# Kernel optimization log

Hardware: AMD Instinct MI355X
Metric: run time of the kernel (lower is better)

## Reference

```python
import jax, jax.numpy as jnp
from jax import lax
import numpy as np

B, T, D, H, C = 256, 2048, 40, 128, 35
LN_EPS = 1e-5


def _uniform(key, shape, scale):
    return jax.random.uniform(key, shape, jnp.float32, -scale, scale)


def setup_inputs() -> dict:
    key = jax.random.key(0)
    ks = jax.random.split(key, 16)
    s = 1.0 / np.sqrt(H)  # PyTorch LSTM init scale
    inp = {
        "x": jax.random.normal(ks[0], (B, T, D), jnp.float32),
        "length": jax.random.randint(ks[1], (B,), 1, T + 1, jnp.int32),
        # layer 0 (input_size=D)
        "W_ih0": _uniform(ks[2], (4 * H, D), s),
        "W_hh0": _uniform(ks[3], (4 * H, H), s),
        "b_ih0": _uniform(ks[4], (4 * H,), s),
        "b_hh0": _uniform(ks[5], (4 * H,), s),
        # layer 1 (input_size=H)
        "W_ih1": _uniform(ks[6], (4 * H, H), s),
        "W_hh1": _uniform(ks[7], (4 * H, H), s),
        "b_ih1": _uniform(ks[8], (4 * H,), s),
        "b_hh1": _uniform(ks[9], (4 * H,), s),
        # LayerNorm + Linear head
        "ln_gamma": jnp.ones((H,), jnp.float32),
        "ln_beta": jnp.zeros((H,), jnp.float32),
        "fc_w": _uniform(ks[10], (C, H), 1.0 / np.sqrt(H)),
        "fc_b": _uniform(ks[11], (C,), 1.0 / np.sqrt(H)),
    }
    return inp


def _lstm_layer(xs, length, W_ih, W_hh, b_ih, b_hh):
    # xs: [T, B, D_in]; masked recurrence emulates pack_padded_sequence:
    # state is frozen for t >= length, so the final h equals the state at
    # each sequence's last valid step.
    Tn, Bn = xs.shape[0], xs.shape[1]
    Hn = W_hh.shape[1]
    h0 = jnp.zeros((Bn, Hn), xs.dtype)
    c0 = jnp.zeros((Bn, Hn), xs.dtype)

    def step(carry, inp):
        h, c = carry
        x_t, t = inp
        gates = x_t @ W_ih.T + b_ih + h @ W_hh.T + b_hh  # [B, 4H]
        i, f, g, o = jnp.split(gates, 4, axis=-1)  # PyTorch gate order i,f,g,o
        i = jax.nn.sigmoid(i)
        f = jax.nn.sigmoid(f)
        g = jnp.tanh(g)
        o = jax.nn.sigmoid(o)
        c_new = f * c + i * g
        h_new = o * jnp.tanh(c_new)
        m = (t < length)[:, None]
        h = jnp.where(m, h_new, h)
        c = jnp.where(m, c_new, c)
        return (h, c), h

    (h_fin, c_fin), hs = lax.scan(step, (h0, c0), (xs, jnp.arange(Tn)))
    return hs, h_fin


def reference(x, length, W_ih0, W_hh0, b_ih0, b_hh0, W_ih1, W_hh1, b_ih1, b_hh1,
              ln_gamma, ln_beta, fc_w, fc_b):
    xs = jnp.transpose(x, (1, 0, 2))  # [T, B, D]
    hs1, _ = _lstm_layer(xs, length, W_ih0, W_hh0, b_ih0, b_hh0)
    _, h_last = _lstm_layer(hs1, length, W_ih1, W_hh1, b_ih1, b_hh1)  # h[-1]: [B, H]
    # LayerNorm over feature dim
    mu = jnp.mean(h_last, axis=-1, keepdims=True)
    var = jnp.mean(jnp.square(h_last - mu), axis=-1, keepdims=True)
    hn = (h_last - mu) * lax.rsqrt(var + LN_EPS) * ln_gamma + ln_beta
    return hn @ fc_w.T + fc_b  # [B, C]
```

## Files before the change

### kernel.cpp

```cpp
#include <hip/hip_runtime.h>

#define Bn 256
#define Tn 2048
#define Dn 40
#define Hn 128
#define Cn 35

typedef _Float16 h2 __attribute__((ext_vector_type(2)));

__device__ __forceinline__ int sdot4(int a, int b, int c) {
#if __has_builtin(__builtin_amdgcn_sdot4)
  return __builtin_amdgcn_sdot4(a, b, c, false);
#else
  int r = c;
#pragma unroll
  for (int i = 0; i < 4; ++i)
    r += ((int)(a << (24 - 8 * i)) >> 24) * ((int)(b << (24 - 8 * i)) >> 24);
  return r;
#endif
}

__device__ __forceinline__ float fdot2f(h2 a, h2 b, float c) {
#if __has_builtin(__builtin_amdgcn_fdot2)
  return __builtin_amdgcn_fdot2(a, b, c, false);
#else
  return c + (float)(a[0]) * (float)(b[0]) + (float)(a[1]) * (float)(b[1]);
#endif
}

__device__ __forceinline__ h2 bch(int u) { return __builtin_bit_cast(h2, u); }

__device__ __forceinline__ int pk2i(float a, float b) {
  h2 r; r[0] = (_Float16)a; r[1] = (_Float16)b;
  return __builtin_bit_cast(int, r);
}

__device__ __forceinline__ float rcpf_(float x) {
#if __has_builtin(__builtin_amdgcn_rcpf)
  return __builtin_amdgcn_rcpf(x);
#else
  return 1.f / x;
#endif
}

__device__ __forceinline__ float sigm(float v) {
  v = fmaxf(fminf(v, 60.f), -60.f);
  return rcpf_(1.f + __expf(-v));
}

__device__ __forceinline__ float tanha(float v) {
  v = fmaxf(fminf(v, 15.f), -15.f);
  const float e = __expf(2.f * v);
  return (e - 1.f) * rcpf_(e + 1.f);
}

__device__ __forceinline__ int q8c(float v) {
  v = fminf(fmaxf(v, -127.f), 127.f);
  return (int)__builtin_rintf(v);
}

__device__ __forceinline__ int pk4(int a, int b, int c, int d) {
  return (a & 255) | ((b & 255) << 8) | ((c & 255) << 16) | (d << 24);
}

__device__ __forceinline__ int dpp_x1(int v) {
  return __builtin_amdgcn_update_dpp(0, v, 0xB1, 0xF, 0xF, true);
}
__device__ __forceinline__ int dpp_x2(int v) {
  return __builtin_amdgcn_update_dpp(0, v, 0x4E, 0xF, 0xF, true);
}

#if __has_builtin(__builtin_amdgcn_global_load_lds)
#define HAVE_GLDS 1
__device__ __forceinline__ void gl_lds16(const float* g, float* l) {
  __builtin_amdgcn_global_load_lds(
      (const __attribute__((address_space(1))) unsigned int*)(const void*)g,
      (__attribute__((address_space(3))) unsigned int*)(void*)l, 16, 0, 0);
}
#endif

__device__ __forceinline__ void quantW128(const float* __restrict__ p,
                                          int* __restrict__ q, float& sc) {
  float m = 1e-30f;
#pragma unroll
  for (int i = 0; i < 32; ++i) {
    const float4 v = reinterpret_cast<const float4*>(p)[i];
    m = fmaxf(m, fmaxf(fmaxf(fabsf(v.x), fabsf(v.y)),
                       fmaxf(fabsf(v.z), fabsf(v.w))));
  }
  const float inv = 127.f / m;
  sc = m * (1.f / 127.f);
#pragma unroll
  for (int i = 0; i < 32; ++i) {
    const float4 v = reinterpret_cast<const float4*>(p)[i];
    q[i] = pk4(q8c(v.x * inv), q8c(v.y * inv), q8c(v.z * inv), q8c(v.w * inv));
  }
}

#define RLST(w) __builtin_amdgcn_readlane(                                  \
    ((w) < 64 ? st0 : (w) < 128 ? st1 : (w) < 192 ? st2 : (w) < 256 ? st3  \
                                                        : st4), (w) & 63)

#define MEMBAR() asm volatile("" ::: "memory")
#define POLL_GE(idx, val, cache)                                             \
  do {                                                                       \
    if ((cache) < (val)) {                                                   \
      do { (cache) = *(volatile int*)&s_flag[idx]; } while ((cache) < (val));\
    }                                                                        \
    MEMBAR();                                                                \
  } while (0)
#define PUBLISH(idx, val)                                                    \
  do {                                                                       \
    MEMBAR();                                                                \
    asm volatile("s_waitcnt lgkmcnt(0)" ::: "memory");                       \
    *(volatile int*)&s_flag[idx] = (val);                                    \
  } while (0)

__global__ __launch_bounds__(256, 1) void lstm2_fused(
    const float* __restrict__ x,
    const int*   __restrict__ length,
    const float* __restrict__ Wih0, const float* __restrict__ Whh0,
    const float* __restrict__ bih0, const float* __restrict__ bhh0,
    const float* __restrict__ Wih1, const float* __restrict__ Whh1,
    const float* __restrict__ bih1, const float* __restrict__ bhh1,
    const float* __restrict__ gam,  const float* __restrict__ bet,
    const float* __restrict__ fcw,  const float* __restrict__ fcb,
    float* __restrict__ out)
{
  __shared__ __align__(16) float s_xraw[160 * 4];
  __shared__ int   s_xh2[320];
  __shared__ float s_xp[2][16][8][64];
  __shared__ float s_term[4][8][64];
  __shared__ int   s_h0q[4][32];
  __shared__ int   s_flag[4];
  __shared__ float s_h1f[128];
  __shared__ float s_hn[128];

  const int tid  = threadIdx.x;
  const int lane = tid & 63;
  const int wv   = tid >> 6;
  const int b    = blockIdx.x;
  const int len  = length[b];

  if (tid < 4) s_flag[tid] = 0;
  __syncthreads();


  if (wv == 0) {
    int q0[32], q1[32], q2[32], q3[32], q4[32], q5[32], q6[32], q7[32];
    float sc[8], bs[8];
    quantW128(Whh0 + (size_t)(lane)       * Hn, q0, sc[0]);
    quantW128(Whh0 + (size_t)(lane + 64)  * Hn, q1, sc[1]);
    quantW128(Whh0 + (size_t)(lane + 128) * Hn, q2, sc[2]);
    quantW128(Whh0 + (size_t)(lane + 192) * Hn, q3, sc[3]);
    quantW128(Whh0 + (size_t)(lane + 256) * Hn, q4, sc[4]);
    quantW128(Whh0 + (size_t)(lane + 320) * Hn, q5, sc[5]);
    quantW128(Whh0 + (size_t)(lane + 384) * Hn, q6, sc[6]);
    quantW128(Whh0 + (size_t)(lane + 448) * Hn, q7, sc[7]);
#pragma unroll
    for (int k = 0; k < 8; ++k) {
      sc[k] *= (1.f / 127.f);
      bs[k] = bih0[lane + 64 * k] + bhh0[lane + 64 * k];
    }
    const int shl = 8 * (lane & 3);
    float cA = 0.f, cB = 0.f;
    int wA = 0, wB = 0;
    int fX = 0, fT = 0;
#pragma unroll 1
    for (int t = 0; t < len; ++t) {
      const int tl = t & 15;
      if (tl == 0) POLL_GE(3, (t >> 4) + 1, fX);
      POLL_GE(1, t - 3, fT);
      const float* xb = &s_xp[(t >> 4) & 1][tl][0][lane];
      float xv0 = xb[0], xv1 = xb[64], xv2 = xb[128], xv3 = xb[192],
            xv4 = xb[256], xv5 = xb[320], xv6 = xb[384], xv7 = xb[448];
      int a0 = 0, a1 = 0, a2 = 0, a3 = 0, a4 = 0, a5 = 0, a6 = 0, a7 = 0;
#pragma unroll
      for (int j = 0; j < 16; ++j) {
        const int s = __builtin_amdgcn_readlane(wA, 4 * j);
        a0 = sdot4(s, q0[j], a0); a1 = sdot4(s, q1[j], a1);
        a2 = sdot4(s, q2[j], a2); a3 = sdot4(s, q3[j], a3);
        a4 = sdot4(s, q4[j], a4); a5 = sdot4(s, q5[j], a5);
        a6 = sdot4(s, q6[j], a6); a7 = sdot4(s, q7[j], a7);
      }
#pragma unroll
      for (int j = 0; j < 16; ++j) {
        const int s = __builtin_amdgcn_readlane(wB, 4 * j);
        a0 = sdot4(s, q0[16 + j], a0); a1 = sdot4(s, q1[16 + j], a1);
        a2 = sdot4(s, q2[16 + j], a2); a3 = sdot4(s, q3[16 + j], a3);
        a4 = sdot4(s, q4[16 + j], a4); a5 = sdot4(s, q5[16 + j], a5);
        a6 = sdot4(s, q6[16 + j], a6); a7 = sdot4(s, q7[16 + j], a7);
      }
      const float gAi = bs[0] + xv0 + (float)a0 * sc[0];
      const float gBi = bs[1] + xv1 + (float)a1 * sc[1];
      const float gAf = bs[2] + xv2 + (float)a2 * sc[2];
      const float gBf = bs[3] + xv3 + (float)a3 * sc[3];
      const float gAg = bs[4] + xv4 + (float)a4 * sc[4];
      const float gBg = bs[5] + xv5 + (float)a5 * sc[5];
      const float gAo = bs[6] + xv6 + (float)a6 * sc[6];
      const float gBo = bs[7] + xv7 + (float)a7 * sc[7];
      cA = sigm(gAf) * cA + sigm(gAi) * tanha(gAg);
      const float hA = sigm(gAo) * tanha(cA);
      cB = sigm(gBf) * cB + sigm(gBi) * tanha(gBg);
      const float hB = sigm(gBo) * tanha(cB);
      int vA = (((int)__builtin_rintf(hA * 127.f)) & 255) << shl;
      int vB = (((int)__builtin_rintf(hB * 127.f)) & 255) << shl;
      vA |= dpp_x1(vA); vA |= dpp_x2(vA);
      vB |= dpp_x1(vB); vB |= dpp_x2(vB);
      wA = vA; wB = vB;
      if ((lane & 3) == 0) {
        s_h0q[t & 3][lane >> 2]        = vA;
        s_h0q[t & 3][16 + (lane >> 2)] = vB;
      }
      fT = *(volatile int*)&s_flag[1];
      PUBLISH(0, t + 1);
    }
  } else if (wv == 1) {
    int q0[32], q1[32], q2[32], q3[32], q4[32], q5[32], q6[32], q7[32];
    float sc[8];
    quantW128(Whh1 + (size_t)(lane)       * Hn, q0, sc[0]);
    quantW128(Whh1 + (size_t)(lane + 64)  * Hn, q1, sc[1]);
    quantW128(Whh1 + (size_t)(lane + 128) * Hn, q2, sc[2]);
    quantW128(Whh1 + (size_t)(lane + 192) * Hn, q3, sc[3]);
    quantW128(Whh1 + (size_t)(lane + 256) * Hn, q4, sc[4]);
    quantW128(Whh1 + (size_t)(lane + 320) * Hn, q5, sc[5]);
    quantW128(Whh1 + (size_t)(lane + 384) * Hn, q6, sc[6]);
    quantW128(Whh1 + (size_t)(lane + 448) * Hn, q7, sc[7]);
#pragma unroll
    for (int k = 0; k < 8; ++k) sc[k] *= (1.f / 127.f);
    const int shl = 8 * (lane & 3);
    float cA = 0.f, cB = 0.f;
    int wA = 0, wB = 0;
    int fT = 0;
#pragma unroll 1
    for (int t = 0; t < len; ++t) {
      POLL_GE(1, t + 1, fT);
      const float* tb = &s_term[t & 3][0][lane];
      float tv0 = tb[0], tv1 = tb[64], tv2 = tb[128], tv3 = tb[192],
            tv4 = tb[256], tv5 = tb[320], tv6 = tb[384], tv7 = tb[448];
      int a0 = 0, a1 = 0, a2 = 0, a3 = 0, a4 = 0, a5 = 0, a6 = 0, a7 = 0;
#pragma unroll
      for (int j = 0; j < 16; ++j) {
        const int s = __builtin_amdgcn_readlane(wA, 4 * j);
        a0 = sdot4(s, q0[j], a0); a1 = sdot4(s, q1[j], a1);
        a2 = sdot4(s, q2[j], a2); a3 = sdot4(s, q3[j], a3);
        a4 = sdot4(s, q4[j], a4); a5 = sdot4(s, q5[j], a5);
        a6 = sdot4(s, q6[j], a6); a7 = sdot4(s, q7[j], a7);
      }
#pragma unroll
      for (int j = 0; j < 16; ++j) {
        const int s = __builtin_amdgcn_readlane(wB, 4 * j);
        a0 = sdot4(s, q0[16 + j], a0); a1 = sdot4(s, q1[16 + j], a1);
        a2 = sdot4(s, q2[16 + j], a2); a3 = sdot4(s, q3[16 + j], a3);
        a4 = sdot4(s, q4[16 + j], a4); a5 = sdot4(s, q5[16 + j], a5);
        a6 = sdot4(s, q6[16 + j], a6); a7 = sdot4(s, q7[16 + j], a7);
      }
      const float gAi = tv0 + (float)a0 * sc[0];
      const float gBi = tv1 + (float)a1 * sc[1];
      const float gAf = tv2 + (float)a2 * sc[2];
      const float gBf = tv3 + (float)a3 * sc[3];
      const float gAg = tv4 + (float)a4 * sc[4];
      const float gBg = tv5 + (float)a5 * sc[5];
      const float gAo = tv6 + (float)a6 * sc[6];
      const float gBo = tv7 + (float)a7 * sc[7];
      cA = sigm(gAf) * cA + sigm(gAi) * tanha(gAg);
      const float hA = sigm(gAo) * tanha(cA);
      cB = sigm(gBf) * cB + sigm(gBi) * tanha(gBg);
      const float hB = sigm(gBo) * tanha(cB);
      if (t == len - 1) { s_h1f[lane] = hA; s_h1f[lane + 64] = hB; }
      int vA = (((int)__builtin_rintf(hA * 127.f)) & 255) << shl;
      int vB = (((int)__builtin_rintf(hB * 127.f)) & 255) << shl;
      vA |= dpp_x1(vA); vA |= dpp_x2(vA);
      vB |= dpp_x1(vB); vB |= dpp_x2(vB);
      wA = vA; wB = vB;
      fT = *(volatile int*)&s_flag[1];
      PUBLISH(2, t + 1);
    }
  } else if (wv == 2) {
    int q0[32], q1[32], q2[32], q3[32], q4[32], q5[32], q6[32], q7[32];
    float sc[8], bs[8];
    quantW128(Wih1 + (size_t)(lane)       * Hn, q0, sc[0]);
    quantW128(Wih1 + (size_t)(lane + 64)  * Hn, q1, sc[1]);
    quantW128(Wih1 + (size_t)(lane + 128) * Hn, q2, sc[2]);
    quantW128(Wih1 + (size_t)(lane + 192) * Hn, q3, sc[3]);
    quantW128(Wih1 + (size_t)(lane + 256) * Hn, q4, sc[4]);
    quantW128(Wih1 + (size_t)(lane + 320) * Hn, q5, sc[5]);
    quantW128(Wih1 + (size_t)(lane + 384) * Hn, q6, sc[6]);
    quantW128(Wih1 + (size_t)(lane + 448) * Hn, q7, sc[7]);
#pragma unroll
    for (int k = 0; k < 8; ++k) {
      sc[k] *= (1.f / 127.f);
      bs[k] = bih1[lane + 64 * k] + bhh1[lane + 64 * k];
    }
    int fL0 = 0, fL1 = 0;
#pragma unroll 1
    for (int t = 0; t < len; ++t) {
      POLL_GE(0, t + 1, fL0);
      POLL_GE(2, t - 3, fL1);
      const int vq = s_h0q[t & 3][lane & 31];
      int a0 = 0, a1 = 0, a2 = 0, a3 = 0, a4 = 0, a5 = 0, a6 = 0, a7 = 0;
#pragma unroll
      for (int j = 0; j < 32; ++j) {
        const int s = __builtin_amdgcn_readlane(vq, j);
        a0 = sdot4(s, q0[j], a0); a1 = sdot4(s, q1[j], a1);
        a2 = sdot4(s, q2[j], a2); a3 = sdot4(s, q3[j], a3);
        a4 = sdot4(s, q4[j], a4); a5 = sdot4(s, q5[j], a5);
        a6 = sdot4(s, q6[j], a6); a7 = sdot4(s, q7[j], a7);
      }
      float* tb = &s_term[t & 3][0][lane];
      tb[0]   = bs[0] + (float)a0 * sc[0];
      tb[64]  = bs[1] + (float)a1 * sc[1];
      tb[128] = bs[2] + (float)a2 * sc[2];
      tb[192] = bs[3] + (float)a3 * sc[3];
      tb[256] = bs[4] + (float)a4 * sc[4];
      tb[320] = bs[5] + (float)a5 * sc[5];
      tb[384] = bs[6] + (float)a6 * sc[6];
      tb[448] = bs[7] + (float)a7 * sc[7];
      fL0 = *(volatile int*)&s_flag[0];
      fL1 = *(volatile int*)&s_flag[2];
      PUBLISH(1, t + 1);
    }
  } else {
    int wp0[20], wp1[20], wp2[20], wp3[20], wp4[20], wp5[20], wp6[20], wp7[20];
    {
      const float* p;
      p = Wih0 + (size_t)(lane)       * Dn;
#pragma unroll
      for (int w = 0; w < 20; ++w) wp0[w] = pk2i(p[2 * w], p[2 * w + 1]);
      p = Wih0 + (size_t)(lane + 64)  * Dn;
#pragma unroll
      for (int w = 0; w < 20; ++w) wp1[w] = pk2i(p[2 * w], p[2 * w + 1]);
      p = Wih0 + (size_t)(lane + 128) * Dn;
#pragma unroll
      for (int w = 0; w < 20; ++w) wp2[w] = pk2i(p[2 * w], p[2 * w + 1]);
      p = Wih0 + (size_t)(lane + 192) * Dn;
#pragma unroll
      for (int w = 0; w < 20; ++w) wp3[w] = pk2i(p[2 * w], p[2 * w + 1]);
      p = Wih0 + (size_t)(lane + 256) * Dn;
#pragma unroll
      for (int w = 0; w < 20; ++w) wp4[w] = pk2i(p[2 * w], p[2 * w + 1]);
      p = Wih0 + (size_t)(lane + 320) * Dn;
#pragma unroll
      for (int w = 0; w < 20; ++w) wp5[w] = pk2i(p[2 * w], p[2 * w + 1]);
      p = Wih0 + (size_t)(lane + 384) * Dn;
#pragma unroll
      for (int w = 0; w < 20; ++w) wp6[w] = pk2i(p[2 * w], p[2 * w + 1]);
      p = Wih0 + (size_t)(lane + 448) * Dn;
#pragma unroll
      for (int w = 0; w < 20; ++w) wp7[w] = pk2i(p[2 * w], p[2 * w + 1]);
    }
    const int nch = (len + 15) >> 4;
    {
      const float* src = x + (size_t)b * Tn * Dn;
#if HAVE_GLDS
      gl_lds16(src + lane * 4,        &s_xraw[lane * 4]);
      gl_lds16(src + (lane + 64) * 4, &s_xraw[(lane + 64) * 4]);
      if (lane < 32)
        gl_lds16(src + (lane + 128) * 4, &s_xraw[(lane + 128) * 4]);
      asm volatile("s_waitcnt vmcnt(0)" ::: "memory");
#else
      *(float4*)&s_xraw[lane * 4] = *(const float4*)(src + lane * 4);
      *(float4*)&s_xraw[(lane + 64) * 4] = *(const float4*)(src + (lane + 64) * 4);
      if (lane < 32)
        *(float4*)&s_xraw[(lane + 128) * 4] = *(const float4*)(src + (lane + 128) * 4);
#endif
      {
        float4 v = *(const float4*)&s_xraw[4 * lane];
        s_xh2[2 * lane] = pk2i(v.x, v.y); s_xh2[2 * lane + 1] = pk2i(v.z, v.w);
        v = *(const float4*)&s_xraw[4 * (lane + 64)];
        s_xh2[2 * (lane + 64)] = pk2i(v.x, v.y);
        s_xh2[2 * (lane + 64) + 1] = pk2i(v.z, v.w);
        if (lane < 32) {
          v = *(const float4*)&s_xraw[4 * (lane + 128)];
          s_xh2[2 * (lane + 128)] = pk2i(v.x, v.y);
          s_xh2[2 * (lane + 128) + 1] = pk2i(v.z, v.w);
        }
      }
    }
    int fL0 = 0;
#pragma unroll 1
    for (int k = 0; k < nch; ++k) {
      const bool more = (k + 1 < nch);
      if (more) {
        const float* src = x + ((size_t)b * Tn + (size_t)(k + 1) * 16) * Dn;
#if HAVE_GLDS
        gl_lds16(src + lane * 4,        &s_xraw[lane * 4]);
        gl_lds16(src + (lane + 64) * 4, &s_xraw[(lane + 64) * 4]);
        if (lane < 32)
          gl_lds16(src + (lane + 128) * 4, &s_xraw[(lane + 128) * 4]);
#else
        *(float4*)&s_xraw[lane * 4] = *(const float4*)(src + lane * 4);
        *(float4*)&s_xraw[(lane + 64) * 4] = *(const float4*)(src + (lane + 64) * 4);
        if (lane < 32)
          *(float4*)&s_xraw[(lane + 128) * 4] = *(const float4*)(src + (lane + 128) * 4);
#endif
      }
      {
        const int* flat = s_xh2;
        const int st0 = flat[lane], st1 = flat[lane + 64],
                  st2 = flat[lane + 128], st3 = flat[lane + 192],
                  st4 = flat[lane + 256];
#pragma unroll 1
        for (int tl = 0; tl < 16; ++tl) {
          float a0 = 0.f, a1 = 0.f, a2 = 0.f, a3 = 0.f,
                a4 = 0.f, a5 = 0.f, a6 = 0.f, a7 = 0.f;
#pragma unroll
          for (int w = 0; w < 20; ++w) {
            const h2 s = bch(RLST(20 * tl + w));
            a0 = fdot2f(s, bch(wp0[w]), a0); a1 = fdot2f(s, bch(wp1[w]), a1);
            a2 = fdot2f(s, bch(wp2[w]), a2); a3 = fdot2f(s, bch(wp3[w]), a3);
            a4 = fdot2f(s, bch(wp4[w]), a4); a5 = fdot2f(s, bch(wp5[w]), a5);
            a6 = fdot2f(s, bch(wp6[w]), a6); a7 = fdot2f(s, bch(wp7[w]), a7);
          }
          float* xb = &s_xp[k & 1][tl][0][lane];
          xb[0] = a0;   xb[64] = a1;  xb[128] = a2; xb[192] = a3;
          xb[256] = a4; xb[320] = a5; xb[384] = a6; xb[448] = a7;
        }
      }
      PUBLISH(3, k + 1);
      if (more) {
        POLL_GE(0, 16 * k, fL0);
#if HAVE_GLDS
        asm volatile("s_waitcnt vmcnt(0)" ::: "memory");
#endif
        float4 v = *(const float4*)&s_xraw[4 * lane];
        s_xh2[2 * lane] = pk2i(v.x, v.y); s_xh2[2 * lane + 1] = pk2i(v.z, v.w);
        v = *(const float4*)&s_xraw[4 * (lane + 64)];
        s_xh2[2 * (lane + 64)] = pk2i(v.x, v.y);
        s_xh2[2 * (lane + 64) + 1] = pk2i(v.z, v.w);
        if (lane < 32) {
          v = *(const float4*)&s_xraw[4 * (lane + 128)];
          s_xh2[2 * (lane + 128)] = pk2i(v.x, v.y);
          s_xh2[2 * (lane + 128) + 1] = pk2i(v.z, v.w);
        }
      }
    }
  }

  __syncthreads();

  if (tid < 64) {
    const float a = s_h1f[tid], d = s_h1f[64 + tid];
    float s = a + d, q = a * a + d * d;
#pragma unroll
    for (int m = 32; m >= 1; m >>= 1) {
      s += __shfl_xor(s, m, 64);
      q += __shfl_xor(q, m, 64);
    }
    const float mu = s * (1.f / 128.f);
    float var = q * (1.f / 128.f) - mu * mu;
    var = fmaxf(var, 0.f);
    const float rstd = rsqrtf(var + 1e-5f);
    s_hn[tid]      = (a - mu) * rstd * gam[tid]      + bet[tid];
    s_hn[64 + tid] = (d - mu) * rstd * gam[64 + tid] + bet[64 + tid];
  }
  __syncthreads();

  if (tid < Cn) {
    float acc = fcb[tid];
    const float* wp = fcw + tid * Hn;
#pragma unroll 4
    for (int k = 0; k < Hn; ++k) acc += s_hn[k] * wp[k];
    out[(size_t)b * Cn + tid] = acc;
  }
}

extern "C" void kernel_launch(void* const* d_in, const int* in_sizes, int n_in,
                              void* d_out, int out_size, void* d_ws, size_t ws_size,
                              hipStream_t stream) {
  (void)in_sizes; (void)n_in; (void)d_ws; (void)ws_size; (void)out_size;
  lstm2_fused<<<dim3(Bn), dim3(256), 0, stream>>>(
      (const float*)d_in[0],  (const int*)d_in[1],
      (const float*)d_in[2],  (const float*)d_in[3],
      (const float*)d_in[4],  (const float*)d_in[5],
      (const float*)d_in[6],  (const float*)d_in[7],
      (const float*)d_in[8],  (const float*)d_in[9],
      (const float*)d_in[10], (const float*)d_in[11],
      (const float*)d_in[12], (const float*)d_in[13],
      (float*)d_out);
}
```

Baseline: 2.494 ms.

## Deepen inter-wave ring buffers to 8 and batch flag publishes

Grows the LDS ring buffers carrying layer-0 h and layer-1 input terms from 4 to 8 slots, relaxes the producer back-pressure checks to match, and has producer waves publish their progress flags every 2 or 4 steps instead of every step. It also drops the opportunistic flag re-reads. The first x chunk is now loaded and converted by all threads before the main barrier rather than serially inside wave 3's prologue. The aim is to cut LDS flag traffic and wait stalls on the serial recurrence critical path. The trade-off is that consumers may wait longer, since they only see progress in batches.

```diff
diff --git a/kernel.cpp b/kernel.cpp
--- a/kernel.cpp
+++ b/kernel.cpp
@@ -130,8 +130,8 @@
   __shared__ __align__(16) float s_xraw[160 * 4];
   __shared__ int   s_xh2[320];
   __shared__ float s_xp[2][16][8][64];
-  __shared__ float s_term[4][8][64];
-  __shared__ int   s_h0q[4][32];
+  __shared__ float s_term[8][8][64];
+  __shared__ int   s_h0q[8][32];
   __shared__ int   s_flag[4];
   __shared__ float s_h1f[128];
   __shared__ float s_hn[128];
@@ -142,7 +142,28 @@
   const int b    = blockIdx.x;
   const int len  = length[b];
 
+  if (wv == 3) {
+    const float* xs = x + (size_t)b * Tn * Dn;
+#if HAVE_GLDS
+    gl_lds16(xs + lane * 4,        &s_xraw[lane * 4]);
+    gl_lds16(xs + (lane + 64) * 4, &s_xraw[(lane + 64) * 4]);
+    if (lane < 32)
+      gl_lds16(xs + (lane + 128) * 4, &s_xraw[(lane + 128) * 4]);
+#else
+    *(float4*)&s_xraw[lane * 4] = *(const float4*)(xs + lane * 4);
+    *(float4*)&s_xraw[(lane + 64) * 4] = *(const float4*)(xs + (lane + 64) * 4);
+    if (lane < 32)
+      *(float4*)&s_xraw[(lane + 128) * 4] = *(const float4*)(xs + (lane + 128) * 4);
+#endif
+  }
+  ((int*)s_h0q)[tid] = 0;
   if (tid < 4) s_flag[tid] = 0;
+  __syncthreads();
+  if (tid < 160) {
+    const float4 v = *(const float4*)&s_xraw[4 * tid];
+    s_xh2[2 * tid]     = pk2i(v.x, v.y);
+    s_xh2[2 * tid + 1] = pk2i(v.z, v.w);
+  }
   __syncthreads();
 
 
@@ -170,7 +191,7 @@
     for (int t = 0; t < len; ++t) {
       const int tl = t & 15;
       if (tl == 0) POLL_GE(3, (t >> 4) + 1, fX);
-      POLL_GE(1, t - 3, fT);
+      POLL_GE(1, t - 7, fT);
       const float* xb = &s_xp[(t >> 4) & 1][tl][0][lane];
       float xv0 = xb[0], xv1 = xb[64], xv2 = xb[128], xv3 = xb[192],
             xv4 = xb[256], xv5 = xb[320], xv6 = xb[384], xv7 = xb[448];
@@ -209,11 +230,10 @@
       vB |= dpp_x1(vB); vB |= dpp_x2(vB);
       wA = vA; wB = vB;
       if ((lane & 3) == 0) {
-        s_h0q[t & 3][lane >> 2]        = vA;
-        s_h0q[t & 3][16 + (lane >> 2)] = vB;
-      }
-      fT = *(volatile int*)&s_flag[1];
-      PUBLISH(0, t + 1);
+        s_h0q[t & 7][lane >> 2]        = vA;
+        s_h0q[t & 7][16 + (lane >> 2)] = vB;
+      }
+      if ((t & 1) || t == len - 1) PUBLISH(0, t + 1);
     }
   } else if (wv == 1) {
     int q0[32], q1[32], q2[32], q3[32], q4[32], q5[32], q6[32], q7[32];
@@ -235,7 +255,7 @@
 #pragma unroll 1
     for (int t = 0; t < len; ++t) {
       POLL_GE(1, t + 1, fT);
-      const float* tb = &s_term[t & 3][0][lane];
+      const float* tb = &s_term[t & 7][0][lane];
       float tv0 = tb[0], tv1 = tb[64], tv2 = tb[128], tv3 = tb[192],
             tv4 = tb[256], tv5 = tb[320], tv6 = tb[384], tv7 = tb[448];
       int a0 = 0, a1 = 0, a2 = 0, a3 = 0, a4 = 0, a5 = 0, a6 = 0, a7 = 0;
@@ -273,8 +293,7 @@
       vA |= dpp_x1(vA); vA |= dpp_x2(vA);
       vB |= dpp_x1(vB); vB |= dpp_x2(vB);
       wA = vA; wB = vB;
-      fT = *(volatile int*)&s_flag[1];
-      PUBLISH(2, t + 1);
+      if (((t & 3) == 3) || t == len - 1) PUBLISH(2, t + 1);
     }
   } else if (wv == 2) {
     int q0[32], q1[32], q2[32], q3[32], q4[32], q5[32], q6[32], q7[32];
@@ -296,8 +315,8 @@
 #pragma unroll 1
     for (int t = 0; t < len; ++t) {
       POLL_GE(0, t + 1, fL0);
-      POLL_GE(2, t - 3, fL1);
-      const int vq = s_h0q[t & 3][lane & 31];
+      POLL_GE(2, t - 7, fL1);
+      const int vq = s_h0q[t & 7][lane & 31];
       int a0 = 0, a1 = 0, a2 = 0, a3 = 0, a4 = 0, a5 = 0, a6 = 0, a7 = 0;
 #pragma unroll
       for (int j = 0; j < 32; ++j) {
@@ -307,18 +326,16 @@
         a4 = sdot4(s, q4[j], a4); a5 = sdot4(s, q5[j], a5);
         a6 = sdot4(s, q6[j], a6); a7 = sdot4(s, q7[j], a7);
       }
-      float* tb = &s_term[t & 3][0][lane];
+      float* tb = &s_term[t & 7][0][lane];
       tb[0]   = bs[0] + (float)a0 * sc[0];
       tb[64]  = bs[1] + (float)a1 * sc[1];
       tb[128] = bs[2] + (float)a2 * sc[2];
       tb[192] = bs[3] + (float)a3 * sc[3];
       tb[256] = bs[4] + (float)a4 * sc[4];
       tb[320] = bs[5] + (float)a5 * sc[5];
+      tb[448] = bs[7] + (float)a7 * sc[7];
       tb[384] = bs[6] + (float)a6 * sc[6];
-      tb[448] = bs[7] + (float)a7 * sc[7];
-      fL0 = *(volatile int*)&s_flag[0];
-      fL1 = *(volatile int*)&s_flag[2];
-      PUBLISH(1, t + 1);
+      if (((t & 3) == 3) || t == len - 1) PUBLISH(1, t + 1);
     }
   } else {
     int wp0[20], wp1[20], wp2[20], wp3[20], wp4[20], wp5[20], wp6[20], wp7[20];
@@ -350,33 +367,6 @@
       for (int w = 0; w < 20; ++w) wp7[w] = pk2i(p[2 * w], p[2 * w + 1]);
     }
     const int nch = (len + 15) >> 4;
-    {
-      const float* src = x + (size_t)b * Tn * Dn;
-#if HAVE_GLDS
-      gl_lds16(src + lane * 4,        &s_xraw[lane * 4]);
-      gl_lds16(src + (lane + 64) * 4, &s_xraw[(lane + 64) * 4]);
-      if (lane < 32)
-        gl_lds16(src + (lane + 128) * 4, &s_xraw[(lane + 128) * 4]);
-      asm volatile("s_waitcnt vmcnt(0)" ::: "memory");
-#else
-      *(float4*)&s_xraw[lane * 4] = *(const float4*)(src + lane * 4);
-      *(float4*)&s_xraw[(lane + 64) * 4] = *(const float4*)(src + (lane + 64) * 4);
-      if (lane < 32)
-        *(float4*)&s_xraw[(lane + 128) * 4] = *(const float4*)(src + (lane + 128) * 4);
-#endif
-      {
-        float4 v = *(const float4*)&s_xraw[4 * lane];
-        s_xh2[2 * lane] = pk2i(v.x, v.y); s_xh2[2 * lane + 1] = pk2i(v.z, v.w);
-        v = *(const float4*)&s_xraw[4 * (lane + 64)];
-        s_xh2[2 * (lane + 64)] = pk2i(v.x, v.y);
-        s_xh2[2 * (lane + 64) + 1] = pk2i(v.z, v.w);
-        if (lane < 32) {
-          v = *(const float4*)&s_xraw[4 * (lane + 128)];
-          s_xh2[2 * (lane + 128)] = pk2i(v.x, v.y);
-          s_xh2[2 * (lane + 128) + 1] = pk2i(v.z, v.w);
-        }
-      }
-    }
     int fL0 = 0;
 #pragma unroll 1
     for (int k = 0; k < nch; ++k) {
```

After: 2.246 ms. 1.11x faster.
